# Kernel optimization log

Hardware: AMD Instinct MI355X
Metric: run time of the kernel (lower is better)

The kernel has to match this reference:

```python
import jax, jax.numpy as jnp
import numpy as np

E, R, D = 4096, 64, 256
LRELU_ALPHA = 0.2

def setup_inputs() -> dict:
    key = jax.random.key(0)
    k1, k2, k3, k4, k5 = jax.random.split(key, 5)
    h = jax.random.normal(k1, (E, D), dtype=jnp.float32)
    r = jax.random.normal(k2, (R, D), dtype=jnp.float32)
    adj_agg = jax.random.normal(k3, (E, R), dtype=jnp.float32)
    lim = 1.0 / np.sqrt(D)
    W_lin = jax.random.uniform(k4, (D, 1), jnp.float32, -lim, lim)  # torch Linear(in_features, 1)
    b_lin = jax.random.uniform(k5, (1,), jnp.float32, -lim, lim)
    return {"h": h, "r": r, "adj_agg": adj_agg, "W_lin": W_lin, "b_lin": b_lin}

def reference(h, r, adj_agg, W_lin, b_lin):
    # h: (E, D), r: (R, D), adj_agg: (E, R)
    adj = jax.nn.softmax(adj_agg, axis=1)
    # (h.repeat(1,R).view(R*E,-1) * r.repeat(E,1)).view(E,R,-1) == h[e]*r[j]
    a_input = h[:, None, :] * r[None, :, :]              # (E, R, D)
    att = adj[:, :, None] * a_input                      # (E, R, D)
    att = jnp.where(att >= 0, att, LRELU_ALPHA * att)    # LeakyReLU
    att_E = jax.nn.softmax(att, axis=0)                  # softmax over entities
    att_R = jax.nn.softmax(att, axis=1)                  # softmax over relations
    # dropout is identity in eval mode
    alpha = (att_R @ W_lin + b_lin).reshape(R, E, 1)     # faithful reshape (not transpose)
    alpha = jax.nn.softmax(alpha, axis=1)
    h_prime = jnp.sum(att_E * h[:, None, :], axis=1)     # (E, D)
    r_prime = jnp.sum(att_R * r[None, :, :], axis=0)     # (R, D)
    return jax.nn.elu(h_prime), jax.nn.elu(r_prime), alpha
```

## Files before the change

kernel.cpp:

```cpp
#include <hip/hip_runtime.h>


#define EN 4096
#define RN 64
#define DN 256
#define JT 16
#define NJT (RN/JT)
#define LOG2E 1.44269504088896340736f
#define CHA 8
#define CHB 8

__device__ __forceinline__ float ex2(float x){ return __builtin_amdgcn_exp2f(x); }

template<int CTRL>
__device__ __forceinline__ float dpp_add(float v){
  int m = __builtin_amdgcn_update_dpp(0, __float_as_int(v), CTRL, 0xf, 0xf, true);
  return v + __int_as_float(m);
}
__device__ __forceinline__ float row16_sum(float v){
  v = dpp_add<0x111>(v);
  v = dpp_add<0x112>(v);
  v = dpp_add<0x114>(v);
  v = dpp_add<0x118>(v);
  return v;
}

__global__ __launch_bounds__(256) void k_adj(const float* __restrict__ adj,
                                             float* __restrict__ s2){
  const int lane = threadIdx.x & 63;
  const int e = blockIdx.x*4 + (threadIdx.x >> 6);
  float a = adj[e*RN + lane];
  float ev = ex2(a * LOG2E);
  float s = ev;
  #pragma unroll
  for(int off = 32; off > 0; off >>= 1) s += __shfl_xor(s, off, 64);
  s2[e*RN + lane] = ev * (LOG2E / s);
}

__global__ __launch_bounds__(256,4) void kA(const float* __restrict__ h,
                                            const float* __restrict__ r,
                                            const float* __restrict__ s2,
                                            float* __restrict__ invlR,
                                            float* __restrict__ lE){
  const int d = threadIdx.x;
  const int e0 = blockIdx.x * CHA;
  __shared__ float s2s[CHA*RN];
  #pragma unroll
  for(int k = 0; k < CHA*RN/256; k++) s2s[k*256 + d] = s2[e0*RN + k*256 + d];
  __syncthreads();

  float lR[CHA];
  #pragma unroll
  for(int ee = 0; ee < CHA; ee++) lR[ee] = 0.f;

  #pragma unroll
  for(int jt = 0; jt < NJT; jt++){
    float rcol[JT], lEacc[JT];
    #pragma unroll
    for(int jj = 0; jj < JT; jj++){ rcol[jj] = r[(jt*JT+jj)*DN + d]; lEacc[jj] = 0.f; }
    #pragma unroll
    for(int ee = 0; ee < CHA; ee++){
      const float he = h[(e0+ee)*DN + d];
      #pragma unroll
      for(int jj = 0; jj < JT; jj++){
        float t  = s2s[ee*RN + jt*JT + jj] * he * rcol[jj];
        float ev = ex2(fmaxf(t, 0.2f*t));
        lR[ee]   += ev;
        lEacc[jj] += ev;
      }
    }
    #pragma unroll
    for(int jj = 0; jj < JT; jj++) atomicAdd(&lE[(jt*JT+jj)*DN + d], lEacc[jj]);
  }
  #pragma unroll
  for(int ee = 0; ee < CHA; ee++) invlR[(e0+ee)*DN + d] = 1.0f / lR[ee];
}

__global__ __launch_bounds__(256,4) void kB(const float* __restrict__ h,
                                            const float* __restrict__ r,
                                            const float* __restrict__ s2,
                                            const float* __restrict__ invlR,
                                            const float* __restrict__ lE,
                                            const float* __restrict__ W,
                                            float* __restrict__ hout,
                                            float* __restrict__ alog,
                                            float* __restrict__ racc_g){
  const int tid  = threadIdx.x;
  const int lane = tid & 63;
  const int grp  = tid >> 4;
  const int e0   = blockIdx.x * CHB;
  __shared__ float s2s[CHB*RN];
  __shared__ float apart[CHB*16*20];
  #pragma unroll
  for(int k = 0; k < CHB*RN/256; k++) s2s[k*256 + tid] = s2[e0*RN + k*256 + tid];
  __syncthreads();

  const float wd = W[tid];
  float sE[CHB];
  #pragma unroll
  for(int ee = 0; ee < CHB; ee++) sE[ee] = 0.f;

  #pragma unroll
  for(int jt = 0; jt < NJT; jt++){
    float rcol[JT], ile[JT], rAcc[JT];
    #pragma unroll
    for(int jj = 0; jj < JT; jj++){
      const int j = jt*JT + jj;
      rcol[jj] = r[j*DN + tid];
      ile[jj]  = 1.0f / lE[j*DN + tid];
      rAcc[jj] = 0.f;
    }
    for(int ee = 0; ee < CHB; ee++){
      const int e = e0 + ee;
      const float he = h[e*DN + tid];
      const float il = invlR[e*DN + tid];
      const float u  = il * wd;
      #pragma unroll
      for(int jg = 0; jg < JT/4; jg++){
        float4 st;
        #pragma unroll
        for(int jj4 = 0; jj4 < 4; jj4++){
          const int jj = jg*4 + jj4;
          float t  = s2s[ee*RN + jt*JT + jj] * he * rcol[jj];
          float ev = ex2(fmaxf(t, 0.2f*t));
          rAcc[jj] = fmaf(ev, il, rAcc[jj]);
          sE[ee]   = fmaf(ev, ile[jj], sE[ee]);
          float rs = row16_sum(ev * u);
          if(jj4==0) st.x = rs; else if(jj4==1) st.y = rs;
          else if(jj4==2) st.z = rs; else st.w = rs;
        }
        if((lane & 15) == 15){
          *reinterpret_cast<float4*>(&apart[(ee*16 + grp)*20 + jg*4]) = st;
        }
      }
    }
    __syncthreads();
    if(tid < CHB*JT){
      const int ee = tid >> 4, jj = tid & 15;
      float sum = 0.f;
      #pragma unroll
      for(int g = 0; g < 16; g++) sum += apart[(ee*16 + g)*20 + jj];
      alog[(e0+ee)*RN + jt*JT + jj] = sum;
    }
    __syncthreads();
    #pragma unroll
    for(int jj = 0; jj < JT; jj++) atomicAdd(&racc_g[(jt*JT+jj)*DN + tid], rAcc[jj]);
  }
  #pragma unroll
  for(int ee = 0; ee < CHB; ee++){
    const int e = e0 + ee;
    float hp = h[e*DN + tid] * sE[ee];
    hout[e*DN + tid] = hp > 0.f ? hp : (ex2(hp*LOG2E) - 1.0f);
  }
}

__global__ __launch_bounds__(256) void kR(const float* __restrict__ r,
                                          const float* __restrict__ racc,
                                          float* __restrict__ rout){
  int i = blockIdx.x*256 + threadIdx.x;
  float v = r[i] * racc[i];
  rout[i] = v > 0.f ? v : (ex2(v*LOG2E) - 1.0f);
}

__global__ __launch_bounds__(256) void kAlpha(const float* __restrict__ alog,
                                              float* __restrict__ aout){
  const int rr = blockIdx.x, tid = threadIdx.x;
  const float* __restrict__ row = alog + rr*EN;
  float exv[16]; float s = 0.f;
  #pragma unroll
  for(int k = 0; k < 16; k++){
    float v = ex2(row[k*256 + tid] * LOG2E);
    exv[k] = v; s += v;
  }
  #pragma unroll
  for(int off = 32; off > 0; off >>= 1) s += __shfl_xor(s, off, 64);
  __shared__ float wsum[4];
  if((tid & 63) == 0) wsum[tid>>6] = s;
  __syncthreads();
  float inv = 1.0f / (wsum[0] + wsum[1] + wsum[2] + wsum[3]);
  float* __restrict__ orow = aout + rr*EN;
  #pragma unroll
  for(int k = 0; k < 16; k++) orow[k*256 + tid] = exv[k] * inv;
}

extern "C" void kernel_launch(void* const* d_in, const int* in_sizes, int n_in,
                              void* d_out, int out_size, void* d_ws, size_t ws_size,
                              hipStream_t stream){
  (void)in_sizes; (void)n_in; (void)out_size; (void)ws_size;
  const float* h   = (const float*)d_in[0];
  const float* r   = (const float*)d_in[1];
  const float* adj = (const float*)d_in[2];
  const float* W   = (const float*)d_in[3];

  float* ws    = (float*)d_ws;
  float* s2    = ws;
  float* invlR = s2 + EN*RN;
  float* lE    = invlR + EN*DN;
  float* racc  = lE + RN*DN;
  float* alog  = racc + RN*DN;

  float* hout = (float*)d_out;
  float* rout = hout + EN*DN;
  float* aout = rout + RN*DN;

  hipMemsetAsync(lE, 0, size_t(RN*DN*2)*sizeof(float), stream);

  k_adj <<<EN/4,      256, 0, stream>>>(adj, s2);
  kA    <<<EN/CHA,    256, 0, stream>>>(h, r, s2, invlR, lE);
  kB    <<<EN/CHB,    256, 0, stream>>>(h, r, s2, invlR, lE, W, hout, alog, racc);
  kR    <<<RN*DN/256, 256, 0, stream>>>(r, racc, rout);
  kAlpha<<<RN,        256, 0, stream>>>(alog, aout);
}
```

Before: 180.9 us.

## Split relation tiles across a second grid dimension in kA and kB

Moves the loop over relation tiles in kA and kB into a second grid dimension, giving four times as many blocks, each handling one 16-relation tile. Per-entity partial sums (row normaliser and h accumulator) are now combined with global atomics into zeroed workspace, and a new elementwise kernel applies the final ELU to h. The goal is more parallelism and fewer serial iterations per block. In exchange it adds atomic traffic on EN*DN buffers, a larger memset, and an extra kernel launch.

After: 213.7 us. 18.1% more time.

```diff
diff --git a/kernel.cpp b/kernel.cpp
--- a/kernel.cpp
+++ b/kernel.cpp
@@ -40,118 +40,109 @@
 __global__ __launch_bounds__(256,4) void kA(const float* __restrict__ h,
                                             const float* __restrict__ r,
                                             const float* __restrict__ s2,
-                                            float* __restrict__ invlR,
+                                            float* __restrict__ lRacc,
                                             float* __restrict__ lE){
-  const int d = threadIdx.x;
+  const int d  = threadIdx.x;
   const int e0 = blockIdx.x * CHA;
-  __shared__ float s2s[CHA*RN];
-  #pragma unroll
-  for(int k = 0; k < CHA*RN/256; k++) s2s[k*256 + d] = s2[e0*RN + k*256 + d];
-  __syncthreads();
-
-  float lR[CHA];
-  #pragma unroll
-  for(int ee = 0; ee < CHA; ee++) lR[ee] = 0.f;
-
-  #pragma unroll
-  for(int jt = 0; jt < NJT; jt++){
-    float rcol[JT], lEacc[JT];
+  const int j0 = blockIdx.y * JT;
+  __shared__ float s2s[CHA*JT];
+  if(d < CHA*JT) s2s[d] = s2[(e0 + (d>>4))*RN + j0 + (d & 15)];
+  __syncthreads();
+
+  float rcol[JT], lEacc[JT];
+  #pragma unroll
+  for(int jj = 0; jj < JT; jj++){ rcol[jj] = r[(j0+jj)*DN + d]; lEacc[jj] = 0.f; }
+
+  #pragma unroll
+  for(int ee = 0; ee < CHA; ee++){
+    const float he = h[(e0+ee)*DN + d];
+    float lRp = 0.f;
     #pragma unroll
-    for(int jj = 0; jj < JT; jj++){ rcol[jj] = r[(jt*JT+jj)*DN + d]; lEacc[jj] = 0.f; }
-    #pragma unroll
-    for(int ee = 0; ee < CHA; ee++){
-      const float he = h[(e0+ee)*DN + d];
-      #pragma unroll
-      for(int jj = 0; jj < JT; jj++){
-        float t  = s2s[ee*RN + jt*JT + jj] * he * rcol[jj];
-        float ev = ex2(fmaxf(t, 0.2f*t));
-        lR[ee]   += ev;
-        lEacc[jj] += ev;
-      }
+    for(int jj = 0; jj < JT; jj++){
+      float t  = s2s[ee*JT + jj] * he * rcol[jj];
+      float ev = ex2(fmaxf(t, 0.2f*t));
+      lRp      += ev;
+      lEacc[jj] += ev;
     }
-    #pragma unroll
-    for(int jj = 0; jj < JT; jj++) atomicAdd(&lE[(jt*JT+jj)*DN + d], lEacc[jj]);
-  }
-  #pragma unroll
-  for(int ee = 0; ee < CHA; ee++) invlR[(e0+ee)*DN + d] = 1.0f / lR[ee];
+    atomicAdd(&lRacc[(e0+ee)*DN + d], lRp);
+  }
+  #pragma unroll
+  for(int jj = 0; jj < JT; jj++) atomicAdd(&lE[(j0+jj)*DN + d], lEacc[jj]);
 }
 
 __global__ __launch_bounds__(256,4) void kB(const float* __restrict__ h,
                                             const float* __restrict__ r,
                                             const float* __restrict__ s2,
-                                            const float* __restrict__ invlR,
+                                            const float* __restrict__ lRacc,
                                             const float* __restrict__ lE,
                                             const float* __restrict__ W,
-                                            float* __restrict__ hout,
+                                            float* __restrict__ hAcc,
                                             float* __restrict__ alog,
                                             float* __restrict__ racc_g){
   const int tid  = threadIdx.x;
   const int lane = tid & 63;
   const int grp  = tid >> 4;
   const int e0   = blockIdx.x * CHB;
-  __shared__ float s2s[CHB*RN];
+  const int j0   = blockIdx.y * JT;
+  __shared__ float s2s[CHB*JT];
   __shared__ float apart[CHB*16*20];
-  #pragma unroll
-  for(int k = 0; k < CHB*RN/256; k++) s2s[k*256 + tid] = s2[e0*RN + k*256 + tid];
+  if(tid < CHB*JT) s2s[tid] = s2[(e0 + (tid>>4))*RN + j0 + (tid & 15)];
   __syncthreads();
 
   const float wd = W[tid];
-  float sE[CHB];
-  #pragma unroll
-  for(int ee = 0; ee < CHB; ee++) sE[ee] = 0.f;
-
-  #pragma unroll
-  for(int jt = 0; jt < NJT; jt++){
-    float rcol[JT], ile[JT], rAcc[JT];
+  float rcol[JT], ile[JT], rAcc[JT];
+  #pragma unroll
+  for(int jj = 0; jj < JT; jj++){
+    rcol[jj] = r[(j0+jj)*DN + tid];
+    ile[jj]  = 1.0f / lE[(j0+jj)*DN + tid];
+    rAcc[jj] = 0.f;
+  }
+
+  #pragma unroll
+  for(int ee = 0; ee < CHB; ee++){
+    const int e = e0 + ee;
+    const float he = h[e*DN + tid];
+    const float il = 1.0f / lRacc[e*DN + tid];
+    const float u  = il * wd;
+    float sEp = 0.f;
     #pragma unroll
-    for(int jj = 0; jj < JT; jj++){
-      const int j = jt*JT + jj;
-      rcol[jj] = r[j*DN + tid];
-      ile[jj]  = 1.0f / lE[j*DN + tid];
-      rAcc[jj] = 0.f;
-    }
-    for(int ee = 0; ee < CHB; ee++){
-      const int e = e0 + ee;
-      const float he = h[e*DN + tid];
-      const float il = invlR[e*DN + tid];
-      const float u  = il * wd;
+    for(int jg = 0; jg < JT/4; jg++){
+      float4 st;
       #pragma unroll
-      for(int jg = 0; jg < JT/4; jg++){
-        float4 st;
-        #pragma unroll
-        for(int jj4 = 0; jj4 < 4; jj4++){
-          const int jj = jg*4 + jj4;
-          float t  = s2s[ee*RN + jt*JT + jj] * he * rcol[jj];
-          float ev = ex2(fmaxf(t, 0.2f*t));
-          rAcc[jj] = fmaf(ev, il, rAcc[jj]);
-          sE[ee]   = fmaf(ev, ile[jj], sE[ee]);
-          float rs = row16_sum(ev * u);
-          if(jj4==0) st.x = rs; else if(jj4==1) st.y = rs;
-          else if(jj4==2) st.z = rs; else st.w = rs;
-        }
-        if((lane & 15) == 15){
-          *reinterpret_cast<float4*>(&apart[(ee*16 + grp)*20 + jg*4]) = st;
-        }
+      for(int jj4 = 0; jj4 < 4; jj4++){
+        const int jj = jg*4 + jj4;
+        float t  = s2s[ee*JT + jj] * he * rcol[jj];
+        float ev = ex2(fmaxf(t, 0.2f*t));
+        rAcc[jj] = fmaf(ev, il, rAcc[jj]);
+        sEp      = fmaf(ev, ile[jj], sEp);
+        float rs = row16_sum(ev * u);
+        if(jj4==0) st.x = rs; else if(jj4==1) st.y = rs;
+        else if(jj4==2) st.z = rs; else st.w = rs;
+      }
+      if((lane & 15) == 15){
+        *reinterpret_cast<float4*>(&apart[(ee*16 + grp)*20 + jg*4]) = st;
       }
     }
-    __syncthreads();
-    if(tid < CHB*JT){
-      const int ee = tid >> 4, jj = tid & 15;
-      float sum = 0.f;
-      #pragma unroll
-      for(int g = 0; g < 16; g++) sum += apart[(ee*16 + g)*20 + jj];
-      alog[(e0+ee)*RN + jt*JT + jj] = sum;
-    }
-    __syncthreads();
+    atomicAdd(&hAcc[e*DN + tid], sEp);
+  }
+  __syncthreads();
+  if(tid < CHB*JT){
+    const int ee = tid >> 4, jj = tid & 15;
+    float sum = 0.f;
     #pragma unroll
-    for(int jj = 0; jj < JT; jj++) atomicAdd(&racc_g[(jt*JT+jj)*DN + tid], rAcc[jj]);
-  }
-  #pragma unroll
-  for(int ee = 0; ee < CHB; ee++){
-    const int e = e0 + ee;
-    float hp = h[e*DN + tid] * sE[ee];
-    hout[e*DN + tid] = hp > 0.f ? hp : (ex2(hp*LOG2E) - 1.0f);
-  }
+    for(int g = 0; g < 16; g++) sum += apart[(ee*16 + g)*20 + jj];
+    alog[(e0+ee)*RN + j0 + jj] = sum;
+  }
+  #pragma unroll
+  for(int jj = 0; jj < JT; jj++) atomicAdd(&racc_g[(j0+jj)*DN + tid], rAcc[jj]);
+}
+
+__global__ __launch_bounds__(256) void kH(const float* __restrict__ h,
+                                          const float* __restrict__ hAcc,
+                                          float* __restrict__ hout){
+  int i = blockIdx.x*256 + threadIdx.x;
+  float v = h[i] * hAcc[i];
+  hout[i] = v > 0.f ? v : (ex2(v*LOG2E) - 1.0f);
 }
 
 __global__ __launch_bounds__(256) void kR(const float* __restrict__ r,
@@ -194,20 +185,23 @@
 
   float* ws    = (float*)d_ws;
   float* s2    = ws;
-  float* invlR = s2 + EN*RN;
-  float* lE    = invlR + EN*DN;
+  float* alog  = s2 + EN*RN;
+  float* lRacc = alog + EN*RN;
+  float* hAcc  = lRacc + EN*DN;
+  float* lE    = hAcc + EN*DN;
   float* racc  = lE + RN*DN;
-  float* alog  = racc + RN*DN;
 
   float* hout = (float*)d_out;
   float* rout = hout + EN*DN;
   float* aout = rout + RN*DN;
 
-  hipMemsetAsync(lE, 0, size_t(RN*DN*2)*sizeof(float), stream);
-
+  hipMemsetAsync(lRacc, 0, size_t(2*EN*DN + 2*RN*DN)*sizeof(float), stream);
+
+  dim3 gridA(EN/CHA, NJT), gridB(EN/CHB, NJT);
   k_adj <<<EN/4,      256, 0, stream>>>(adj, s2);
-  kA    <<<EN/CHA,    256, 0, stream>>>(h, r, s2, invlR, lE);
-  kB    <<<EN/CHB,    256, 0, stream>>>(h, r, s2, invlR, lE, W, hout, alog, racc);
+  kA    <<<gridA,     256, 0, stream>>>(h, r, s2, lRacc, lE);
+  kB    <<<gridB,     256, 0, stream>>>(h, r, s2, lRacc, lE, W, hAcc, alog, racc);
+  kH    <<<EN*DN/256, 256, 0, stream>>>(h, hAcc, hout);
   kR    <<<RN*DN/256, 256, 0, stream>>>(r, racc, rout);
   kAlpha<<<RN,        256, 0, stream>>>(alog, aout);
 }
```
